# Kernel optimization log

Measured on AMD Instinct MI355X. Metric: run time of the kernel, lower is better.

Reference implementation:

```python
import jax, jax.numpy as jnp
import numpy as np

B, N, C = 4, 2048, 1024
H = 16
HD = C // H
SCALE = HD ** -0.5


def setup_inputs() -> dict:
    key = jax.random.key(0)
    k1, k2, k3, k4 = jax.random.split(key, 4)
    x = jax.random.normal(k1, (B, N, C), dtype=jnp.float32)
    w_qkv = jax.random.normal(k2, (3 * C, C), dtype=jnp.float32) * (C ** -0.5)
    w_proj = jax.random.normal(k3, (C, C), dtype=jnp.float32) * (C ** -0.5)
    b_proj = jax.random.normal(k4, (C,), dtype=jnp.float32) * 0.01
    return {"x": x, "w_qkv": w_qkv, "w_proj": w_proj, "b_proj": b_proj}


def reference(x, w_qkv, w_proj, b_proj):
    qkv = jnp.einsum('bnc,dc->bnd', x, w_qkv)
    qkv = qkv.reshape(B, N, 3, H, HD).transpose(2, 0, 3, 1, 4)
    q, k, v = qkv[0], qkv[1], qkv[2]
    # scaled dot-product attention with explicit softmax (dropout p=0 -> identity)
    attn = jnp.einsum('bhqd,bhkd->bhqk', q, k) * SCALE
    attn = jax.nn.softmax(attn, axis=-1)
    out = jnp.einsum('bhqk,bhkd->bhqd', attn, v)
    out = out.transpose(0, 2, 1, 3).reshape(B, N, C)
    # output projection
    return jnp.einsum('bnc,dc->bnd', out, w_proj) + b_proj
```

## Files before the change

### kernel.cpp

```cpp
#include <hip/hip_runtime.h>

typedef unsigned short u16;
typedef unsigned int u32;
typedef __bf16 bf16x8 __attribute__((ext_vector_type(8)));
typedef __bf16 bf16x4 __attribute__((ext_vector_type(4)));
typedef short s16x4 __attribute__((ext_vector_type(4)));
typedef float f32x4 __attribute__((ext_vector_type(4)));
typedef float f32x16 __attribute__((ext_vector_type(16)));
typedef unsigned int u32x2 __attribute__((ext_vector_type(2)));
typedef unsigned int u32x4 __attribute__((ext_vector_type(4)));

struct __align__(8) u16x4 { u16 x, y, z, w; };

__device__ __forceinline__ void async_copy16(const void* g, void* l) {
  __builtin_amdgcn_global_load_lds(
      (__attribute__((address_space(1))) void*)g,
      (__attribute__((address_space(3))) void*)l, 16, 0, 0);
}

__device__ __forceinline__ u16 f2bf(float f) {
  unsigned u = __builtin_bit_cast(unsigned, f);
  u = (u + 0x7FFFu + ((u >> 16) & 1u)) >> 16;
  return (u16)u;
}
__device__ __forceinline__ float bf2f(u16 h) {
  unsigned u = ((unsigned)h) << 16;
  return __builtin_bit_cast(float, u);
}

__device__ __forceinline__ float fast_exp2(float x) {
  return __builtin_amdgcn_exp2f(x);
}
__device__ __forceinline__ float fast_rcp(float x) {
  return __builtin_amdgcn_rcpf(x);
}

__device__ __forceinline__ f32x4 mfma32(bf16x8 a, bf16x8 b, f32x4 c) {
  return __builtin_amdgcn_mfma_f32_16x16x32_bf16(a, b, c, 0, 0, 0);
}

__device__ __forceinline__ u32 cvt_pk_bf16(float lo, float hi) {
  u32 r;
  asm("v_cvt_pk_bf16_f32 %0, %1, %2" : "=v"(r) : "v"(lo), "v"(hi));
  return r;
}

#define CEXP 0.18033688011112042f

__global__ void detect_mode(const u32* __restrict__ probe, int* __restrict__ flag) {
  __shared__ int cnt[256];
  int t = threadIdx.x;
  int c = 0;
#pragma unroll
  for (int j = 0; j < 16; ++j) {
    u32 v = probe[t + j * 256];
    unsigned e = (v >> 7) & 0xFFu;
    c += (e >= 100u && e <= 130u) ? 1 : 0;
  }
  cnt[t] = c;
  __syncthreads();
  for (int s = 128; s > 0; s >>= 1) {
    if (t < s) cnt[t] += cnt[t + s];
    __syncthreads();
  }
  if (t == 0) *flag = (cnt[0] * 2 > 4096) ? 1 : 0;
}

__global__ void convert_in(const void* __restrict__ src, u16* __restrict__ dst,
                           const int* __restrict__ flag, int n) {
  int mode = *flag;
  int i = (blockIdx.x * blockDim.x + threadIdx.x) * 8;
  if (i >= n) return;
  if (mode == 1) {
    *(uint4*)(dst + i) = *(const uint4*)((const u16*)src + i);
  } else {
    const float* s = (const float*)src;
    float4 a = *(const float4*)(s + i);
    float4 b = *(const float4*)(s + i + 4);
    uint4 o;
    o.x = (u32)f2bf(a.x) | ((u32)f2bf(a.y) << 16);
    o.y = (u32)f2bf(a.z) | ((u32)f2bf(a.w) << 16);
    o.z = (u32)f2bf(b.x) | ((u32)f2bf(b.y) << 16);
    o.w = (u32)f2bf(b.z) | ((u32)f2bf(b.w) << 16);
    *(uint4*)(dst + i) = o;
  }
}

template<int NJ>
__global__ __launch_bounds__(512, 2) void gemm_bt(
    const u16* __restrict__ A, const u16* __restrict__ Bm,
    u16* __restrict__ C, u16* __restrict__ vT, const u16* __restrict__ bias,
    float* __restrict__ outF, const int* __restrict__ flagp,
    int K, int ldc)
{
  __shared__ __align__(16) char lds[65536 + NJ * 16384];

  const int t = threadIdx.x;
  const int lane = t & 63, wave = t >> 6;
  const int quad = lane >> 4, l16 = lane & 15;
  const int wn = wave & 3, wm = wave >> 2;

  const int nwg = gridDim.x * gridDim.y;
  int bid = blockIdx.y * gridDim.x + blockIdx.x;
  bid = (bid & 7) * (nwg >> 3) + (bid >> 3);
  const int rowbase = (bid / gridDim.x) * 256;
  const int colbase = (bid % gridDim.x) * (NJ * 64);

  const int srow = t >> 3;
  const int scol = ((t & 7) << 4) ^ ((srow & 7) << 4);
  const int wlds = wave << 10;

  const u16* Arow = A + (size_t)(rowbase + srow) * K + (scol >> 1);
  const u16* Brow = Bm + (size_t)(colbase + srow) * K + (scol >> 1);

  auto stageA = [&](int kb_, int buf_) {
#pragma unroll
    for (int q = 0; q < 4; ++q)
      async_copy16(Arow + (size_t)kb_ * 64 + (size_t)q * 64 * K,
                   lds + buf_ * 32768 + q * 8192 + wlds);
  };
  auto stageB = [&](int kb_, int buf_) {
#pragma unroll
    for (int q = 0; q < NJ; ++q)
      async_copy16(Brow + (size_t)kb_ * 64 + (size_t)q * 64 * K,
                   lds + 65536 + buf_ * (NJ * 8192) + q * 8192 + wlds);
  };

  f32x4 acc[8][NJ] = {};

  const int swzl = (l16 & 7) << 4;
  const int c0 = (quad * 16) ^ swzl;
  const int c1 = (64 + quad * 16) ^ swzl;
  const char* Ard = lds + (size_t)(wm * 128 + l16) * 128;
  const char* Brd = lds + 65536 + (size_t)(wn * (NJ * 16) + l16) * 128;

  stageA(0, 0); stageB(0, 0);
  stageA(1, 1); stageB(1, 1);
  if constexpr (NJ == 3) asm volatile("s_waitcnt vmcnt(7)" ::: "memory");
  else                   asm volatile("s_waitcnt vmcnt(6)" ::: "memory");
  __builtin_amdgcn_s_barrier();

  const int nkb = K >> 6;
  for (int kb = 0; kb < nkb; ++kb) {
    const int cur = kb & 1;
    const char* Ab = Ard + cur * 32768;
    const char* Bb = Brd + cur * (NJ * 8192);
    bf16x8 aR[4][2], bR[NJ][2];

#pragma unroll
    for (int i = 0; i < 4; ++i) {
      aR[i][0] = *(const bf16x8*)(Ab + i * 2048 + c0);
      aR[i][1] = *(const bf16x8*)(Ab + i * 2048 + c1);
    }
#pragma unroll
    for (int j = 0; j < NJ; ++j) {
      bR[j][0] = *(const bf16x8*)(Bb + j * 2048 + c0);
      bR[j][1] = *(const bf16x8*)(Bb + j * 2048 + c1);
    }
    __builtin_amdgcn_s_barrier();
    __builtin_amdgcn_s_setprio(1);
#pragma unroll
    for (int i = 0; i < 4; ++i)
#pragma unroll
      for (int j = 0; j < NJ; ++j) {
        acc[i][j] = mfma32(aR[i][0], bR[j][0], acc[i][j]);
        acc[i][j] = mfma32(aR[i][1], bR[j][1], acc[i][j]);
      }
    __builtin_amdgcn_s_setprio(0);
    __builtin_amdgcn_s_barrier();
    if (kb + 2 < nkb) stageB(kb + 2, cur);

#pragma unroll
    for (int i = 0; i < 4; ++i) {
      aR[i][0] = *(const bf16x8*)(Ab + 8192 + i * 2048 + c0);
      aR[i][1] = *(const bf16x8*)(Ab + 8192 + i * 2048 + c1);
    }
    __builtin_amdgcn_s_barrier();
    __builtin_amdgcn_s_setprio(1);
#pragma unroll
    for (int i = 0; i < 4; ++i)
#pragma unroll
      for (int j = 0; j < NJ; ++j) {
        acc[4 + i][j] = mfma32(aR[i][0], bR[j][0], acc[4 + i][j]);
        acc[4 + i][j] = mfma32(aR[i][1], bR[j][1], acc[4 + i][j]);
      }
    __builtin_amdgcn_s_setprio(0);
    __builtin_amdgcn_s_barrier();

    if (kb + 2 < nkb) {
      stageA(kb + 2, cur);
      if constexpr (NJ == 3) asm volatile("s_waitcnt vmcnt(7)" ::: "memory");
      else                   asm volatile("s_waitcnt vmcnt(6)" ::: "memory");
      __builtin_amdgcn_s_barrier();
    } else if (kb + 1 < nkb) {
      asm volatile("s_waitcnt vmcnt(0)" ::: "memory");
      __builtin_amdgcn_s_barrier();
    }
  }

  const bool f32out = (flagp != nullptr) && (*flagp == 0);
#pragma unroll
  for (int nj = 0; nj < NJ; ++nj) {
    int cg = colbase + wn * (NJ * 16) + nj * 16 + l16;
    if (vT != nullptr && cg >= 2048) {
#pragma unroll
      for (int mi = 0; mi < 8; ++mi) {
        int rg = rowbase + wm * 128 + mi * 16 + quad * 4;
        int b = rg >> 11, n = rg & 2047;
        size_t idx = ((size_t)(b * 1024 + (cg - 2048))) * 2048 + n;
        u16x4 pk;
        pk.x = f2bf(acc[mi][nj][0]); pk.y = f2bf(acc[mi][nj][1]);
        pk.z = f2bf(acc[mi][nj][2]); pk.w = f2bf(acc[mi][nj][3]);
        *(u16x4*)(vT + idx) = pk;
      }
    } else {
      const float scl = (vT != nullptr && cg < 1024) ? CEXP : 1.0f;
      float bv = bias ? bf2f(bias[cg]) : 0.0f;
#pragma unroll
      for (int mi = 0; mi < 8; ++mi) {
#pragma unroll
        for (int r = 0; r < 4; ++r) {
          int rg = rowbase + wm * 128 + mi * 16 + quad * 4 + r;
          float val = acc[mi][nj][r] * scl + bv;
          if (f32out) outF[(size_t)rg * ldc + cg] = val;
          else        C[(size_t)rg * ldc + cg] = f2bf(val);
        }
      }
    }
  }
}

__global__ __launch_bounds__(256, 4) void attn_fwd(
    const u16* __restrict__ qk, const u16* __restrict__ vT, u16* __restrict__ outp)
{
  __shared__ __align__(16) char sm[32768];

  const int t = threadIdx.x;
  const int lane = t & 63, wave = t >> 6;
  const int l31 = lane & 31, h32 = lane >> 5;
  const int bh = blockIdx.x, b = bh >> 4, h = bh & 15;
  const int qtile = blockIdx.y;
  const size_t row0 = (size_t)b * 2048;
  const int qb = qtile * 128 + wave * 32;

  bf16x8 qf[4];
  {
    const u16* qp = qk + (row0 + qb + l31) * 2048 + h * 64 + h32 * 8;
#pragma unroll
    for (int s = 0; s < 4; ++s)
      qf[s] = *(const bf16x8*)(qp + s * 16);
  }

  const u16* Kg[2]; const u16* Vg[2]; unsigned loff[2];
#pragma unroll
  for (int q = 0; q < 2; ++q) {
    int si = q * 256 + t;
    int srow = si >> 3;
    int scolb = ((si & 7) << 4) ^ ((srow & 7) << 4);
    Kg[q] = qk + (row0 + srow) * 2048 + 1024 + h * 64 + (scolb >> 1);
    Vg[q] = vT + ((size_t)(b * 1024 + h * 64 + srow)) * 2048 + (scolb >> 1);
    loff[q] = q * 4096 + wave * 1024;
  }

#pragma unroll
  for (int q = 0; q < 2; ++q) {
    async_copy16(Kg[q], sm + loff[q]);
    async_copy16(Vg[q], sm + 16384 + loff[q]);
  }

  const int swz = (lane & 7) << 4;
  int cswz[4];
#pragma unroll
  for (int s = 0; s < 4; ++s) cswz[s] = (s * 32 + h32 * 16) ^ swz;
  const int rowb = l31 * 128;

  f32x16 o2[2] = {};
  float lsum = 0.0f;

  for (int kb = 0; kb < 32; ++kb) {
    const int cur = kb & 1, nxt = cur ^ 1;
    __syncthreads();
    if (kb < 31) {
#pragma unroll
      for (int q = 0; q < 2; ++q) {
        async_copy16(Kg[q] + (size_t)(kb + 1) * 64 * 2048, sm + nxt * 8192 + loff[q]);
        async_copy16(Vg[q] + (kb + 1) * 64, sm + 16384 + nxt * 8192 + loff[q]);
      }
    }
    const char* Kb = sm + cur * 8192;
    const char* Vb = sm + 16384 + cur * 8192;

#pragma unroll
    for (int kh = 0; kh < 2; ++kh) {
      f32x16 s2 = {};
      __builtin_amdgcn_s_setprio(1);
#pragma unroll
      for (int s = 0; s < 4; ++s) {
        bf16x8 kf = *(const bf16x8*)(Kb + kh * 4096 + rowb + cswz[s]);
        s2 = __builtin_amdgcn_mfma_f32_32x32x16_bf16(kf, qf[s], s2, 0, 0, 0);
      }
      __builtin_amdgcn_s_setprio(0);

      u32 u[8];
#pragma unroll
      for (int w = 0; w < 8; ++w) {
        float p0 = fast_exp2(s2[2 * w]);
        float p1 = fast_exp2(s2[2 * w + 1]);
        lsum += p0 + p1;
        u[w] = cvt_pk_bf16(p0, p1);
      }

      u32x2 r02 = __builtin_amdgcn_permlane32_swap(u[0], u[2], false, false);
      u32x2 r13 = __builtin_amdgcn_permlane32_swap(u[1], u[3], false, false);
      u32x2 r46 = __builtin_amdgcn_permlane32_swap(u[4], u[6], false, false);
      u32x2 r57 = __builtin_amdgcn_permlane32_swap(u[5], u[7], false, false);
      u32x4 fa0v; fa0v.x = r02.x; fa0v.y = r13.x; fa0v.z = r02.y; fa0v.w = r13.y;
      u32x4 fa1v; fa1v.x = r46.x; fa1v.y = r57.x; fa1v.z = r46.y; fa1v.w = r57.y;
      bf16x8 fa0 = __builtin_bit_cast(bf16x8, fa0v);
      bf16x8 fa1 = __builtin_bit_cast(bf16x8, fa1v);

      __builtin_amdgcn_s_setprio(1);
#pragma unroll
      for (int eb = 0; eb < 2; ++eb) {
        bf16x8 v0 = *(const bf16x8*)(Vb + eb * 4096 + rowb + cswz[kh * 2 + 0]);
        o2[eb] = __builtin_amdgcn_mfma_f32_32x32x16_bf16(fa0, v0, o2[eb], 0, 0, 0);
        bf16x8 v1 = *(const bf16x8*)(Vb + eb * 4096 + rowb + cswz[kh * 2 + 1]);
        o2[eb] = __builtin_amdgcn_mfma_f32_32x32x16_bf16(fa1, v1, o2[eb], 0, 0, 0);
      }
      __builtin_amdgcn_s_setprio(0);
    }
  }

  lsum += __shfl_xor(lsum, 32, 64);
  float inv = fast_rcp(lsum);

#pragma unroll
  for (int r = 0; r < 16; ++r) {
    int qr = (r & 3) + 8 * (r >> 2) + 4 * h32;
    float iv = __shfl(inv, qr, 64);
    size_t base = (row0 + qb + qr) * 1024 + h * 64 + l31;
    outp[base]      = f2bf(o2[0][r] * iv);
    outp[base + 32] = f2bf(o2[1][r] * iv);
  }
}

extern "C" void kernel_launch(void* const* d_in, const int* in_sizes, int n_in,
                              void* d_out, int out_size, void* d_ws, size_t ws_size,
                              hipStream_t stream) {
  (void)in_sizes; (void)n_in; (void)out_size; (void)ws_size;
  const void* x_in     = d_in[0];
  const void* wqkv_in  = d_in[1];
  const void* wproj_in = d_in[2];
  const void* bproj_in = d_in[3];

  u16* qkbuf  = (u16*)d_ws;
  u16* vT     = qkbuf + 16777216;
  u16* xb     = vT + 8388608;
  u16* wqkvb  = xb + 8388608;
  int* flag   = (int*)(wqkvb + 3145728);
  u16* attn   = xb;
  u16* wprojb = vT;
  u16* bprojb = vT + 1048576;

  detect_mode<<<1, 256, 0, stream>>>((const u32*)wqkv_in, flag);
  convert_in<<<4096, 256, 0, stream>>>(x_in, xb, flag, 8388608);
  convert_in<<<1536, 256, 0, stream>>>(wqkv_in, wqkvb, flag, 3145728);

  gemm_bt<3><<<dim3(16, 32), 512, 0, stream>>>(xb, wqkvb, qkbuf, vT, nullptr,
                                               nullptr, nullptr, 1024, 2048);
  attn_fwd<<<dim3(64, 16), 256, 0, stream>>>(qkbuf, vT, attn);

  convert_in<<<512, 256, 0, stream>>>(wproj_in, wprojb, flag, 1048576);
  convert_in<<<1, 256, 0, stream>>>(bproj_in, bprojb, flag, 1024);

  gemm_bt<2><<<dim3(8, 32), 512, 0, stream>>>(attn, wprojb, (u16*)d_out, nullptr,
                                              bprojb, (float*)d_out, flag, 1024, 1024);
}
```

Before: 267.5 us.

## Shrink GEMM tiles to 128x128, enlarge attention blocks, compute row sums via MFMA

The GEMM drops the 256-row, 512-thread template in favour of a uniform 128x128 tile with 256 threads and a simpler double-buffered staging loop, launched over more workgroups. The attention kernel now uses 512-thread blocks covering 256 queries, so each block loads every K/V tile once for more waves, with explicit waitcnt/barrier handling. The softmax denominator is accumulated by extra MFMAs against a ones vector instead of scalar adds and shuffles. Smaller GEMM tiles lower arithmetic intensity per LDS load, and the extra MFMAs add matrix work in the attention loop.

```diff
diff --git a/kernel.cpp b/kernel.cpp
--- a/kernel.cpp
+++ b/kernel.cpp
@@ -86,25 +86,24 @@
   }
 }
 
-template<int NJ>
-__global__ __launch_bounds__(512, 2) void gemm_bt(
+__global__ __launch_bounds__(256, 2) void gemm_bt(
     const u16* __restrict__ A, const u16* __restrict__ Bm,
     u16* __restrict__ C, u16* __restrict__ vT, const u16* __restrict__ bias,
     float* __restrict__ outF, const int* __restrict__ flagp,
     int K, int ldc)
 {
-  __shared__ __align__(16) char lds[65536 + NJ * 16384];
+  __shared__ __align__(16) char lds[65536];
 
   const int t = threadIdx.x;
   const int lane = t & 63, wave = t >> 6;
   const int quad = lane >> 4, l16 = lane & 15;
-  const int wn = wave & 3, wm = wave >> 2;
+  const int wn = wave & 1, wm = wave >> 1;
 
   const int nwg = gridDim.x * gridDim.y;
   int bid = blockIdx.y * gridDim.x + blockIdx.x;
   bid = (bid & 7) * (nwg >> 3) + (bid >> 3);
-  const int rowbase = (bid / gridDim.x) * 256;
-  const int colbase = (bid % gridDim.x) * (NJ * 64);
+  const int rowbase = (bid / gridDim.x) * 128;
+  const int colbase = (bid % gridDim.x) * 128;
 
   const int srow = t >> 3;
   const int scol = ((t & 7) << 4) ^ ((srow & 7) << 4);
@@ -113,114 +112,94 @@
   const u16* Arow = A + (size_t)(rowbase + srow) * K + (scol >> 1);
   const u16* Brow = Bm + (size_t)(colbase + srow) * K + (scol >> 1);
 
-  auto stageA = [&](int kb_, int buf_) {
-#pragma unroll
-    for (int q = 0; q < 4; ++q)
-      async_copy16(Arow + (size_t)kb_ * 64 + (size_t)q * 64 * K,
-                   lds + buf_ * 32768 + q * 8192 + wlds);
+  auto stage = [&](int kb_, int buf_) {
+#pragma unroll
+    for (int q = 0; q < 4; ++q) {
+      async_copy16(Arow + (size_t)kb_ * 64 + (size_t)q * 32 * K,
+                   lds + buf_ * 16384 + q * 4096 + wlds);
+      async_copy16(Brow + (size_t)kb_ * 64 + (size_t)q * 32 * K,
+                   lds + 32768 + buf_ * 16384 + q * 4096 + wlds);
+    }
   };
-  auto stageB = [&](int kb_, int buf_) {
-#pragma unroll
-    for (int q = 0; q < NJ; ++q)
-      async_copy16(Brow + (size_t)kb_ * 64 + (size_t)q * 64 * K,
-                   lds + 65536 + buf_ * (NJ * 8192) + q * 8192 + wlds);
-  };
-
-  f32x4 acc[8][NJ] = {};
+
+  f32x4 acc[4][4] = {};
 
   const int swzl = (l16 & 7) << 4;
   const int c0 = (quad * 16) ^ swzl;
   const int c1 = (64 + quad * 16) ^ swzl;
-  const char* Ard = lds + (size_t)(wm * 128 + l16) * 128;
-  const char* Brd = lds + 65536 + (size_t)(wn * (NJ * 16) + l16) * 128;
-
-  stageA(0, 0); stageB(0, 0);
-  stageA(1, 1); stageB(1, 1);
-  if constexpr (NJ == 3) asm volatile("s_waitcnt vmcnt(7)" ::: "memory");
-  else                   asm volatile("s_waitcnt vmcnt(6)" ::: "memory");
+  const char* Ard = lds + (size_t)(wm * 64 + l16) * 128;
+  const char* Brd = lds + 32768 + (size_t)(wn * 64 + l16) * 128;
+
+  stage(0, 0);
+  stage(1, 1);
+  asm volatile("s_waitcnt vmcnt(8)" ::: "memory");
   __builtin_amdgcn_s_barrier();
 
   const int nkb = K >> 6;
   for (int kb = 0; kb < nkb; ++kb) {
     const int cur = kb & 1;
-    const char* Ab = Ard + cur * 32768;
-    const char* Bb = Brd + cur * (NJ * 8192);
-    bf16x8 aR[4][2], bR[NJ][2];
-
+    const char* Ab = Ard + cur * 16384;
+    const char* Bb = Brd + cur * 16384;
+
+    bf16x8 aR[4][2], bR[4][2];
 #pragma unroll
     for (int i = 0; i < 4; ++i) {
       aR[i][0] = *(const bf16x8*)(Ab + i * 2048 + c0);
       aR[i][1] = *(const bf16x8*)(Ab + i * 2048 + c1);
     }
 #pragma unroll
-    for (int j = 0; j < NJ; ++j) {
+    for (int j = 0; j < 4; ++j) {
       bR[j][0] = *(const bf16x8*)(Bb + j * 2048 + c0);
       bR[j][1] = *(const bf16x8*)(Bb + j * 2048 + c1);
     }
-    __builtin_amdgcn_s_barrier();
     __builtin_amdgcn_s_setprio(1);
 #pragma unroll
     for (int i = 0; i < 4; ++i)
 #pragma unroll
-      for (int j = 0; j < NJ; ++j) {
+      for (int j = 0; j < 4; ++j) {
         acc[i][j] = mfma32(aR[i][0], bR[j][0], acc[i][j]);
         acc[i][j] = mfma32(aR[i][1], bR[j][1], acc[i][j]);
       }
     __builtin_amdgcn_s_setprio(0);
+
+    if (kb + 1 >= nkb) break;
     __builtin_amdgcn_s_barrier();
-    if (kb + 2 < nkb) stageB(kb + 2, cur);
-
-#pragma unroll
-    for (int i = 0; i < 4; ++i) {
-      aR[i][0] = *(const bf16x8*)(Ab + 8192 + i * 2048 + c0);
-      aR[i][1] = *(const bf16x8*)(Ab + 8192 + i * 2048 + c1);
+    if (kb + 2 < nkb) {
+      stage(kb + 2, cur);
+      asm volatile("s_waitcnt vmcnt(8)" ::: "memory");
+    } else {
+      asm volatile("s_waitcnt vmcnt(0)" ::: "memory");
     }
     __builtin_amdgcn_s_barrier();
-    __builtin_amdgcn_s_setprio(1);
-#pragma unroll
-    for (int i = 0; i < 4; ++i)
-#pragma unroll
-      for (int j = 0; j < NJ; ++j) {
-        acc[4 + i][j] = mfma32(aR[i][0], bR[j][0], acc[4 + i][j]);
-        acc[4 + i][j] = mfma32(aR[i][1], bR[j][1], acc[4 + i][j]);
-      }
-    __builtin_amdgcn_s_setprio(0);
-    __builtin_amdgcn_s_barrier();
-
-    if (kb + 2 < nkb) {
-      stageA(kb + 2, cur);
-      if constexpr (NJ == 3) asm volatile("s_waitcnt vmcnt(7)" ::: "memory");
-      else                   asm volatile("s_waitcnt vmcnt(6)" ::: "memory");
-      __builtin_amdgcn_s_barrier();
-    } else if (kb + 1 < nkb) {
-      asm volatile("s_waitcnt vmcnt(0)" ::: "memory");
-      __builtin_amdgcn_s_barrier();
-    }
-  }
-
-  const bool f32out = (flagp != nullptr) && (*flagp == 0);
-#pragma unroll
-  for (int nj = 0; nj < NJ; ++nj) {
-    int cg = colbase + wn * (NJ * 16) + nj * 16 + l16;
-    if (vT != nullptr && cg >= 2048) {
-#pragma unroll
-      for (int mi = 0; mi < 8; ++mi) {
-        int rg = rowbase + wm * 128 + mi * 16 + quad * 4;
-        int b = rg >> 11, n = rg & 2047;
+  }
+
+  if (vT != nullptr && colbase >= 2048) {
+#pragma unroll
+    for (int mi = 0; mi < 4; ++mi) {
+      int rg = rowbase + wm * 64 + mi * 16 + quad * 4;
+      int b = rg >> 11, n = rg & 2047;
+#pragma unroll
+      for (int nj = 0; nj < 4; ++nj) {
+        int cg = colbase + wn * 64 + nj * 16 + l16;
         size_t idx = ((size_t)(b * 1024 + (cg - 2048))) * 2048 + n;
         u16x4 pk;
         pk.x = f2bf(acc[mi][nj][0]); pk.y = f2bf(acc[mi][nj][1]);
         pk.z = f2bf(acc[mi][nj][2]); pk.w = f2bf(acc[mi][nj][3]);
         *(u16x4*)(vT + idx) = pk;
       }
-    } else {
-      const float scl = (vT != nullptr && cg < 1024) ? CEXP : 1.0f;
+    }
+  } else {
+    const bool f32out = (flagp != nullptr) && (*flagp == 0);
+    const float scl = (vT != nullptr && colbase < 1024) ? CEXP : 1.0f;
+#pragma unroll
+    for (int nj = 0; nj < 4; ++nj) {
+      int cg = colbase + wn * 64 + nj * 16 + l16;
       float bv = bias ? bf2f(bias[cg]) : 0.0f;
 #pragma unroll
-      for (int mi = 0; mi < 8; ++mi) {
+      for (int mi = 0; mi < 4; ++mi) {
 #pragma unroll
         for (int r = 0; r < 4; ++r) {
-          int rg = rowbase + wm * 128 + mi * 16 + quad * 4 + r;
+          int rg = rowbase + wm * 64 + mi * 16 + quad * 4 + r;
           float val = acc[mi][nj][r] * scl + bv;
           if (f32out) outF[(size_t)rg * ldc + cg] = val;
           else        C[(size_t)rg * ldc + cg] = f2bf(val);
@@ -230,7 +209,7 @@
   }
 }
 
-__global__ __launch_bounds__(256, 4) void attn_fwd(
+__global__ __launch_bounds__(512, 2) void attn_fwd(
     const u16* __restrict__ qk, const u16* __restrict__ vT, u16* __restrict__ outp)
 {
   __shared__ __align__(16) char sm[32768];
@@ -241,7 +220,7 @@
   const int bh = blockIdx.x, b = bh >> 4, h = bh & 15;
   const int qtile = blockIdx.y;
   const size_t row0 = (size_t)b * 2048;
-  const int qb = qtile * 128 + wave * 32;
+  const int qb = qtile * 256 + wave * 32;
 
   bf16x8 qf[4];
   {
@@ -251,22 +230,14 @@
       qf[s] = *(const bf16x8*)(qp + s * 16);
   }
 
-  const u16* Kg[2]; const u16* Vg[2]; unsigned loff[2];
-#pragma unroll
-  for (int q = 0; q < 2; ++q) {
-    int si = q * 256 + t;
-    int srow = si >> 3;
-    int scolb = ((si & 7) << 4) ^ ((srow & 7) << 4);
-    Kg[q] = qk + (row0 + srow) * 2048 + 1024 + h * 64 + (scolb >> 1);
-    Vg[q] = vT + ((size_t)(b * 1024 + h * 64 + srow)) * 2048 + (scolb >> 1);
-    loff[q] = q * 4096 + wave * 1024;
-  }
-
-#pragma unroll
-  for (int q = 0; q < 2; ++q) {
-    async_copy16(Kg[q], sm + loff[q]);
-    async_copy16(Vg[q], sm + 16384 + loff[q]);
-  }
+  const int srow = t >> 3;
+  const int scolb = ((t & 7) << 4) ^ ((srow & 7) << 4);
+  const u16* Kg = qk + (row0 + srow) * 2048 + 1024 + h * 64 + (scolb >> 1);
+  const u16* Vg = vT + ((size_t)(b * 1024 + h * 64 + srow)) * 2048 + (scolb >> 1);
+  const unsigned loff = (unsigned)wave << 10;
+
+  async_copy16(Kg, sm + loff);
+  async_copy16(Vg, sm + 16384 + loff);
 
   const int swz = (lane & 7) << 4;
   int cswz[4];
@@ -274,19 +245,25 @@
   for (int s = 0; s < 4; ++s) cswz[s] = (s * 32 + h32 * 16) ^ swz;
   const int rowb = l31 * 128;
 
+  u32x4 onev; onev.x = 0x3F803F80u; onev.y = 0x3F803F80u;
+  onev.z = 0x3F803F80u; onev.w = 0x3F803F80u;
+  const bf16x8 ones = __builtin_bit_cast(bf16x8, onev);
+
   f32x16 o2[2] = {};
-  float lsum = 0.0f;
+  f32x16 o3 = {};
 
   for (int kb = 0; kb < 32; ++kb) {
     const int cur = kb & 1, nxt = cur ^ 1;
-    __syncthreads();
+    __builtin_amdgcn_s_barrier();
     if (kb < 31) {
-#pragma unroll
-      for (int q = 0; q < 2; ++q) {
-        async_copy16(Kg[q] + (size_t)(kb + 1) * 64 * 2048, sm + nxt * 8192 + loff[q]);
-        async_copy16(Vg[q] + (kb + 1) * 64, sm + 16384 + nxt * 8192 + loff[q]);
-      }
-    }
+      async_copy16(Kg + (size_t)(kb + 1) * 64 * 2048, sm + nxt * 8192 + loff);
+      async_copy16(Vg + (kb + 1) * 64, sm + 16384 + nxt * 8192 + loff);
+      asm volatile("s_waitcnt vmcnt(2)" ::: "memory");
+    } else {
+      asm volatile("s_waitcnt vmcnt(0)" ::: "memory");
+    }
+    __builtin_amdgcn_s_barrier();
+
     const char* Kb = sm + cur * 8192;
     const char* Vb = sm + 16384 + cur * 8192;
 
@@ -306,7 +283,6 @@
       for (int w = 0; w < 8; ++w) {
         float p0 = fast_exp2(s2[2 * w]);
         float p1 = fast_exp2(s2[2 * w + 1]);
-        lsum += p0 + p1;
         u[w] = cvt_pk_bf16(p0, p1);
       }
 
@@ -327,17 +303,16 @@
         bf16x8 v1 = *(const bf16x8*)(Vb + eb * 4096 + rowb + cswz[kh * 2 + 1]);
         o2[eb] = __builtin_amdgcn_mfma_f32_32x32x16_bf16(fa1, v1, o2[eb], 0, 0, 0);
       }
+      o3 = __builtin_amdgcn_mfma_f32_32x32x16_bf16(fa0, ones, o3, 0, 0, 0);
+      o3 = __builtin_amdgcn_mfma_f32_32x32x16_bf16(fa1, ones, o3, 0, 0, 0);
       __builtin_amdgcn_s_setprio(0);
     }
   }
-
-  lsum += __shfl_xor(lsum, 32, 64);
-  float inv = fast_rcp(lsum);
 
 #pragma unroll
   for (int r = 0; r < 16; ++r) {
     int qr = (r & 3) + 8 * (r >> 2) + 4 * h32;
-    float iv = __shfl(inv, qr, 64);
+    float iv = fast_rcp(o3[r]);
     size_t base = (row0 + qb + qr) * 1024 + h * 64 + l31;
     outp[base]      = f2bf(o2[0][r] * iv);
     outp[base + 32] = f2bf(o2[1][r] * iv);
@@ -366,13 +341,13 @@
   convert_in<<<4096, 256, 0, stream>>>(x_in, xb, flag, 8388608);
   convert_in<<<1536, 256, 0, stream>>>(wqkv_in, wqkvb, flag, 3145728);
 
-  gemm_bt<3><<<dim3(16, 32), 512, 0, stream>>>(xb, wqkvb, qkbuf, vT, nullptr,
-                                               nullptr, nullptr, 1024, 2048);
-  attn_fwd<<<dim3(64, 16), 256, 0, stream>>>(qkbuf, vT, attn);
+  gemm_bt<<<dim3(24, 64), 256, 0, stream>>>(xb, wqkvb, qkbuf, vT, nullptr,
+                                            nullptr, nullptr, 1024, 2048);
+  attn_fwd<<<dim3(64, 8), 512, 0, stream>>>(qkbuf, vT, attn);
 
   convert_in<<<512, 256, 0, stream>>>(wproj_in, wprojb, flag, 1048576);
   convert_in<<<1, 256, 0, stream>>>(bproj_in, bprojb, flag, 1024);
 
-  gemm_bt<2><<<dim3(8, 32), 512, 0, stream>>>(attn, wprojb, (u16*)d_out, nullptr,
-                                              bprojb, (float*)d_out, flag, 1024, 1024);
-}
+  gemm_bt<<<dim3(8, 64), 256, 0, stream>>>(attn, wprojb, (u16*)d_out, nullptr,
+                                           bprojb, (float*)d_out, flag, 1024, 1024);
+}
```

After: 264.0 us. Within noise of the previous version (-1.3%).
